# Kernel optimization log

Hardware: AMD Instinct MI355X
Metric: run time of the kernel (lower is better)

Reference implementation:

```python
import math
import jax, jax.numpy as jnp
import numpy as np

STEP = 0.1
EPS = 1e-12


def _laplacian(src, dst, n):
    # dense symmetric-normalized Laplacian from COO edge list (symmetrized, 0/1 weights)
    A = jnp.zeros((n, n), dtype=jnp.float32).at[src, dst].set(1.0)
    A = jnp.maximum(A, A.T)
    deg = A.sum(axis=1)
    dinv = jnp.where(deg > 0, 1.0 / jnp.sqrt(jnp.maximum(deg, 1e-12)), 0.0)
    return jnp.eye(n, dtype=jnp.float32) - dinv[:, None] * A * dinv[None, :]


def _filter_bank(L, bs):
    # rational band-pass bank centered at b in arange(0,2.1,STEP):
    # D_b = sqrt(2)*a * inv((L - b I)^4 + a I),  a = (STEP/2)^4
    n = L.shape[0]
    a = (STEP / 2.0) ** 4
    I = jnp.eye(n, dtype=L.dtype)

    def one(b):
        M1 = L - b * I
        P2 = M1 @ M1
        P4 = P2 @ P2
        return math.sqrt(2.0) * a * jnp.linalg.inv(P4 + a * I)

    return jax.vmap(one)(bs)  # [F, n, n]


def _cdist_mean(e):
    # mean pairwise euclidean distance, safe sqrt on the zero diagonal
    d2 = jnp.sum((e[:, None, :] - e[None, :, :]) ** 2, axis=-1)
    d = jnp.sqrt(jnp.where(d2 > 0, d2, 1.0))
    return jnp.where(d2 > 0, d, 0.0).mean()


def setup_inputs() -> dict:
    key = jax.random.key(0)
    k1, k2, k3, k4, k5 = jax.random.split(key, 5)
    B, N, F0, R, E = 64, 128, 32, 1118, 512
    return {
        "x": jax.random.normal(k1, (B, N, F0), dtype=jnp.float32),
        "random_signal": jax.random.normal(k2, (B, N, R), dtype=jnp.float32),
        "C": jax.random.normal(k3, (21, 1), dtype=jnp.float32),
        "edge_src": jax.random.randint(k4, (B, E), 0, N),
        "edge_dst": jax.random.randint(k5, (B, E), 0, N),
        "num_classes": 4,
    }


def reference(x, random_signal, C, edge_src, edge_dst, num_classes):
    B, N, _ = x.shape
    R = random_signal.shape[-1]
    # torch.normal(0, sqrt(1/R)) random signal concatenated to features
    feats = jnp.concatenate([x, random_signal * math.sqrt(1.0 / R)], axis=-1)  # [B,N,F0+R]
    bs = jnp.arange(0.0, 2.1, STEP, dtype=jnp.float32)  # [21]
    Cn = C / jnp.maximum(jnp.linalg.norm(C, axis=0, keepdims=True), EPS)  # F.normalize(C, dim=0)

    def per_graph(src, dst, xg):
        L = _laplacian(src, dst, N)
        D = _filter_bank(L, bs)                      # [F,N,N]
        L_hat = jnp.einsum('fnm,f->nm', D, Cn[:, 0])  # D.permute(1,2,0) @ C, squeezed
        A_hat = jnp.eye(N, dtype=xg.dtype) - L_hat
        y = A_hat @ xg                                # [N, F0+R]
        z = y / jnp.maximum(jnp.linalg.norm(y, axis=1, keepdims=True), EPS)
        logits = z @ z.T                              # decode_all on normalized x
        sp = -jnp.abs(logits).sum() / (N * N)         # -||logits||_1 / n^2
        return y.mean(axis=0), sp

    emb, sp_terms = jax.vmap(per_graph)(edge_src, edge_dst, feats)  # [B,D], [B]

    # faithful repeated in-loop division: s_{i+1} = (s_i + t_i)/B  =>  sum_i t_i * B^{-(B-i)}
    i = jnp.arange(B, dtype=jnp.float32)
    w = jnp.exp(-(B - i) * jnp.log(float(B)))
    sparsity_fwd = jnp.sum(sp_terms * w)

    # labels y = arange(B) % num_classes; one positive group (class members) and
    # one negative group (non-members) per class
    idx = np.arange(B)
    hl1 = jnp.float32(0.0)
    hl2 = jnp.float32(0.0)
    for c in range(num_classes):
        pos = jnp.asarray(idx[idx % num_classes == c])
        neg = jnp.asarray(idx[idx % num_classes != c])
        beta = 1.0 / num_classes + 1e-13  # one group per class
        hl1 = hl1 + (-_cdist_mean(emb[neg])) / beta
        hl2 = hl2 + _cdist_mean(emb[pos])

    Fk = C.shape[0]
    dims = jnp.sqrt(jnp.float32(Fk))
    c_l1 = jnp.sum(jnp.abs(C), axis=0)
    c_l2 = jnp.maximum(jnp.linalg.norm(C, axis=0), EPS)
    sparsity_c = jnp.mean((dims - c_l1 / c_l2) / (dims - 1.0))

    return sparsity_c + hl2 + hl1 + sparsity_fwd
```

## Files before the change

### kernel.cpp

```cpp
#include <hip/hip_runtime.h>
#include <math.h>

#define NN 128
#define SM 129
#define RS 132
#define SS 17
#define SD 130
#define EP 132

typedef double d4 __attribute__((ext_vector_type(4)));

__global__ __launch_bounds__(512, 1) void k1_lap_pow2(
    const int* __restrict__ src, const int* __restrict__ dst,
    int E, float* __restrict__ Lout, double* __restrict__ L2) {
  extern __shared__ float smf[];
  float* dinv = smf + NN * SM;
  const int g   = blockIdx.x;
  const int tid = threadIdx.x;
  const int wv = tid >> 6, ln = tid & 63;
  const int m  = ln & 15, kq = ln >> 4;

  int rIdx[4], cIdx[4];
  {
    d4 z = {0.0, 0.0, 0.0, 0.0};
    d4 pr = __builtin_amdgcn_mfma_f64_16x16x4f64((double)m, 1.0, z, 0, 0, 0);
    d4 pc = __builtin_amdgcn_mfma_f64_16x16x4f64(1.0, (double)m, z, 0, 0, 0);
#pragma unroll
    for (int r = 0; r < 4; ++r) {
      rIdx[r] = ((int)(pr[r] * 0.25 + 0.5)) & 15;
      cIdx[r] = ((int)(pc[r] * 0.25 + 0.5)) & 15;
    }
  }

  for (int e = tid; e < NN * NN; e += 512) {
    int i = e >> 7, j = e & 127;
    smf[i * SM + j] = 0.f;
  }
  __syncthreads();
  const int* s = src + (size_t)g * E;
  const int* d = dst + (size_t)g * E;
  for (int e = tid; e < E; e += 512) {
    int a = s[e], b = d[e];
    smf[a * SM + b] = 1.f;
    smf[b * SM + a] = 1.f;
  }
  __syncthreads();
  if (tid < NN) {
    float acc = 0.f;
    for (int j = 0; j < NN; ++j) acc += smf[tid * SM + j];
    dinv[tid] = (acc > 0.f) ? (float)(1.0 / sqrt((double)acc)) : 0.f;
  }
  __syncthreads();
  float* Lg = Lout + (size_t)g * NN * NN;
  for (int e = tid; e < NN * NN; e += 512) {
    int i = e >> 7, j = e & 127;
    float v = ((i == j) ? 1.f : 0.f) - dinv[i] * dinv[j] * smf[i * SM + j];
    Lg[e] = v;
    smf[i * SM + j] = v;
  }
  __syncthreads();

  d4 acc[8];
#pragma unroll
  for (int cb = 0; cb < 8; ++cb) {
    acc[cb][0] = 0.0; acc[cb][1] = 0.0; acc[cb][2] = 0.0; acc[cb][3] = 0.0;
  }
  for (int kc = 0; kc < 32; ++kc) {
    double a = (double)smf[(16 * wv + m) * SM + 4 * kc + kq];
#pragma unroll
    for (int cb = 0; cb < 8; ++cb) {
      double b = (double)smf[(4 * kc + kq) * SM + 16 * cb + m];
      acc[cb] = __builtin_amdgcn_mfma_f64_16x16x4f64(a, b, acc[cb], 0, 0, 0);
    }
  }
  double* out = L2 + (size_t)g * NN * NN;
#pragma unroll
  for (int cb = 0; cb < 8; ++cb)
#pragma unroll
    for (int r = 0; r < 4; ++r)
      out[(16 * wv + rIdx[r]) * NN + 16 * cb + cIdx[r]] = acc[cb][r];
}

__global__ __launch_bounds__(512, 1) void k1_pow34(
    const float* __restrict__ L, const double* __restrict__ L2,
    double* __restrict__ L3, double* __restrict__ L4) {
  extern __shared__ double Bs[];
  const int bid = blockIdx.x;
  const int g = bid >> 1, job = bid & 1;
  const int tid = threadIdx.x;
  const int wv = tid >> 6, ln = tid & 63;
  const int m  = ln & 15, kq = ln >> 4;

  int rIdx[4], cIdx[4];
  {
    d4 z = {0.0, 0.0, 0.0, 0.0};
    d4 pr = __builtin_amdgcn_mfma_f64_16x16x4f64((double)m, 1.0, z, 0, 0, 0);
    d4 pc = __builtin_amdgcn_mfma_f64_16x16x4f64(1.0, (double)m, z, 0, 0, 0);
#pragma unroll
    for (int r = 0; r < 4; ++r) {
      rIdx[r] = ((int)(pr[r] * 0.25 + 0.5)) & 15;
      cIdx[r] = ((int)(pc[r] * 0.25 + 0.5)) & 15;
    }
  }

  const float*  Lg  = L  + (size_t)g * NN * NN;
  const double* L2g = L2 + (size_t)g * NN * NN;
  if (job == 0) {
    for (int e = tid; e < NN * NN; e += 512) {
      int i = e >> 7, j = e & 127;
      Bs[i * SD + j] = (double)Lg[e];
    }
  } else {
    for (int e = tid; e < NN * NN; e += 512) {
      int i = e >> 7, j = e & 127;
      Bs[i * SD + j] = L2g[e];
    }
  }
  __syncthreads();

  d4 acc[8];
#pragma unroll
  for (int cb = 0; cb < 8; ++cb) {
    acc[cb][0] = 0.0; acc[cb][1] = 0.0; acc[cb][2] = 0.0; acc[cb][3] = 0.0;
  }
  for (int kc = 0; kc < 32; ++kc) {
    double a = L2g[(16 * wv + m) * NN + 4 * kc + kq];
#pragma unroll
    for (int cb = 0; cb < 8; ++cb) {
      double b = Bs[(4 * kc + kq) * SD + 16 * cb + m];
      acc[cb] = __builtin_amdgcn_mfma_f64_16x16x4f64(a, b, acc[cb], 0, 0, 0);
    }
  }
  double* out = (job == 0 ? L3 : L4) + (size_t)g * NN * NN;
#pragma unroll
  for (int cb = 0; cb < 8; ++cb)
#pragma unroll
    for (int r = 0; r < 4; ++r)
      out[(16 * wv + rIdx[r]) * NN + 16 * cb + cIdx[r]] = acc[cb][r];
}

__global__ __launch_bounds__(512, 4) void k2_filter(
    const float* __restrict__ L, const double* __restrict__ L2,
    const double* __restrict__ L3, const double* __restrict__ L4,
    const float* __restrict__ C, int NF, float* __restrict__ W) {
  extern __shared__ char smraw[];
  double* Rp  = (double*)smraw;
  double* Scd = (double*)(smraw + 16 * RS * 8);
  double* Pv  = (double*)(smraw + 16 * RS * 8 + 8 * 16 * SS * 8);

  const int bid = blockIdx.x;
  const int g = bid / NF, f = bid % NF;
  const int tid = threadIdx.x;
  const int wv = tid >> 6, ln = tid & 63;
  const int m  = ln & 15, kq = ln >> 4;
  double* S = Scd + wv * 16 * SS;

  double csum = 0.0;
  for (int q = 0; q < NF; ++q) { double c = (double)C[q]; csum += c * c; }
  double cn = sqrt(csum); if (cn < 1e-12) cn = 1e-12;
  const double a4 = 6.25e-6;
  const double coef = 1.4142135623730951 * a4 * ((double)C[f] / cn);
  const float  bf = (float)((double)f * 0.1);
  const double bb = (double)bf;
  const double c3 = -4.0 * bb;
  const double c2 = 6.0 * bb * bb;
  const double c1 = -4.0 * bb * bb * bb;
  const double c0 = bb * bb * bb * bb + a4;

  int rIdx[4], cIdx[4];
  {
    d4 z = {0.0, 0.0, 0.0, 0.0};
    d4 pr = __builtin_amdgcn_mfma_f64_16x16x4f64((double)m, 1.0, z, 0, 0, 0);
    d4 pc = __builtin_amdgcn_mfma_f64_16x16x4f64(1.0, (double)m, z, 0, 0, 0);
#pragma unroll
    for (int r = 0; r < 4; ++r) {
      rIdx[r] = ((int)(pr[r] * 0.25 + 0.5)) & 15;
      cIdx[r] = ((int)(pc[r] * 0.25 + 0.5)) & 15;
    }
  }

  const float*  Lg  = L  + (size_t)g * NN * NN;
  const double* L2g = L2 + (size_t)g * NN * NN;
  const double* L3g = L3 + (size_t)g * NN * NN;
  const double* L4g = L4 + (size_t)g * NN * NN;
  d4 T[8];
#pragma unroll
  for (int cb = 0; cb < 8; ++cb)
#pragma unroll
    for (int r = 0; r < 4; ++r) {
      int i = 16 * wv + rIdx[r], j = 16 * cb + cIdx[r];
      int idx = i * NN + j;
      double v = L4g[idx];
      v = fma(c3, L3g[idx], v);
      v = fma(c2, L2g[idx], v);
      v = fma(c1, (double)Lg[idx], v);
      if (i == j) v += c0;
      T[cb][r] = v;
    }

#pragma unroll 1
  for (int t = 0; t < 8; ++t) {
    if (wv == t) {
#pragma unroll
      for (int cb = 0; cb < 8; ++cb)
#pragma unroll
        for (int r = 0; r < 4; ++r)
          Rp[rIdx[r] * RS + 16 * cb + cIdx[r]] = T[cb][r];
    }
    __syncthreads();

    if (wv == t) {
      double sr[4];
#pragma unroll
      for (int r = 0; r < 4; ++r) sr[r] = Rp[(4 * r + kq) * RS + 16 * t + m];
#pragma unroll
      for (int k = 0; k < 16; ++k) {
        const int kr = k >> 2, kl = k & 3;
        double pv   = __shfl(sr[kr], 16 * kl + k);
        double rowv = __shfl(sr[kr], 16 * kl + m);
        double cv[4];
#pragma unroll
        for (int r = 0; r < 4; ++r) cv[r] = __shfl(sr[r], 16 * kq + k);
        double dp = 1.0 / pv;
#pragma unroll
        for (int r = 0; r < 4; ++r) {
          int i = 4 * r + kq;
          double nv;
          if (i == k)      nv = (m == k) ? dp : rowv * dp;
          else if (m == k) nv = -cv[r] * dp;
          else             nv = fma(-(cv[r] * dp), rowv, sr[r]);
          sr[r] = nv;
        }
      }
#pragma unroll
      for (int r = 0; r < 4; ++r) Pv[(4 * r + kq) * SS + m] = sr[r];
    }
    __syncthreads();

#pragma unroll
    for (int cb = 0; cb < 8; ++cb) {
      if (cb != t) continue;
      if (wv == t) {
#pragma unroll
        for (int r = 0; r < 4; ++r) T[cb][r] = Pv[rIdx[r] * SS + cIdx[r]];
      } else {
#pragma unroll
        for (int r = 0; r < 4; ++r) S[rIdx[r] * SS + cIdx[r]] = T[cb][r];
        __builtin_amdgcn_wave_barrier();
        d4 ncv = {0.0, 0.0, 0.0, 0.0};
#pragma unroll
        for (int kc = 0; kc < 4; ++kc) {
          double a = S[m * SS + 4 * kc + kq];
          double b = -Pv[(4 * kc + kq) * SS + m];
          ncv = __builtin_amdgcn_mfma_f64_16x16x4f64(a, b, ncv, 0, 0, 0);
        }
        T[cb] = ncv;
        __builtin_amdgcn_wave_barrier();
#pragma unroll
        for (int r = 0; r < 4; ++r) S[rIdx[r] * SS + cIdx[r]] = T[cb][r];
      }
    }
    __builtin_amdgcn_wave_barrier();

    const double* asrc = (wv == t) ? Pv : S;
#pragma unroll
    for (int cb = 0; cb < 8; ++cb) {
      if (cb == t) continue;
      d4 acc;
      if (wv == t) { acc[0] = 0.0; acc[1] = 0.0; acc[2] = 0.0; acc[3] = 0.0; }
      else         { acc = T[cb]; }
#pragma unroll
      for (int kc = 0; kc < 4; ++kc) {
        double a = asrc[m * SS + 4 * kc + kq];
        double b = Rp[(4 * kc + kq) * RS + 16 * cb + m];
        acc = __builtin_amdgcn_mfma_f64_16x16x4f64(a, b, acc, 0, 0, 0);
      }
      T[cb] = acc;
    }
    __syncthreads();
  }

  float* Wg = W + (size_t)g * NN * NN;
#pragma unroll
  for (int cb = 0; cb < 8; ++cb)
#pragma unroll
    for (int r = 0; r < 4; ++r)
      atomicAdd(&Wg[(16 * wv + rIdx[r]) * NN + 16 * cb + cIdx[r]],
                (float)(coef * T[cb][r]));
}

__global__ __launch_bounds__(512, 1) void k3_fused(
    const float* __restrict__ x, const float* __restrict__ rs,
    const float* __restrict__ W, float* __restrict__ G,
    float* __restrict__ emb, int F0, int R, int DTOT, int NCH,
    float rscale) {
  extern __shared__ float sm3[];
  float* ldsW = sm3;
  float* ldsX = sm3 + NN * SM;
  const int bid = blockIdx.x;
  const int g = bid / NCH;
  const int c = bid % NCH;
  const int d0 = c * 128;
  const int tid = threadIdx.x, tr = tid >> 4, tc = tid & 15;

  const float* Wg = W + (size_t)g * NN * NN;
  for (int e = tid; e < NN * NN; e += 512) {
    int k = e >> 7, i = e & 127;
    ldsW[k * SM + i] = Wg[e];
  }
  const float* xg = x + (size_t)g * NN * F0;
  const float* rg = rs + (size_t)g * NN * R;
  for (int e = tid; e < NN * NN; e += 512) {
    int k = e >> 7, dl = e & 127;
    int d = d0 + dl;
    float v = 0.f;
    if (d < DTOT) v = (d < F0) ? xg[k * F0 + d] : rg[k * R + (d - F0)] * rscale;
    ldsX[k * SM + dl] = v;
  }
  __syncthreads();

  float acc[4][8];
#pragma unroll
  for (int v = 0; v < 4; ++v)
#pragma unroll
    for (int u = 0; u < 8; ++u) acc[v][u] = 0.f;
  for (int k = 0; k < NN; ++k) {
    float wvv[4], xv[8];
#pragma unroll
    for (int v = 0; v < 4; ++v) wvv[v] = ldsW[k * SM + 4 * tr + v];
#pragma unroll
    for (int u = 0; u < 8; ++u) xv[u] = ldsX[k * SM + tc + 16 * u];
#pragma unroll
    for (int v = 0; v < 4; ++v)
#pragma unroll
      for (int u = 0; u < 8; ++u) acc[v][u] = fmaf(wvv[v], xv[u], acc[v][u]);
  }
#pragma unroll
  for (int v = 0; v < 4; ++v)
#pragma unroll
    for (int u = 0; u < 8; ++u)
      acc[v][u] = ldsX[(4 * tr + v) * SM + tc + 16 * u] - acc[v][u];
  __syncthreads();

#pragma unroll
  for (int v = 0; v < 4; ++v)
#pragma unroll
    for (int u = 0; u < 8; ++u)
      ldsW[(tc + 16 * u) * SM + 4 * tr + v] = acc[v][u];
#pragma unroll
  for (int u = 0; u < 8; ++u) {
    float s = 0.f;
#pragma unroll
    for (int v = 0; v < 4; ++v) s += acc[v][u];
    ldsX[tr * EP + tc + 16 * u] = s;
  }
  __syncthreads();

  float gg[4][8];
#pragma unroll
  for (int v = 0; v < 4; ++v)
#pragma unroll
    for (int u = 0; u < 8; ++u) gg[v][u] = 0.f;
  for (int dl = 0; dl < NN; ++dl) {
    float av[4], bv[8];
#pragma unroll
    for (int v = 0; v < 4; ++v) av[v] = ldsW[dl * SM + 4 * tr + v];
#pragma unroll
    for (int u = 0; u < 8; ++u) bv[u] = ldsW[dl * SM + tc + 16 * u];
#pragma unroll
    for (int v = 0; v < 4; ++v)
#pragma unroll
      for (int u = 0; u < 8; ++u) gg[v][u] = fmaf(av[v], bv[u], gg[v][u]);
  }
  float* Gg = G + (size_t)g * NN * NN;
#pragma unroll
  for (int v = 0; v < 4; ++v)
#pragma unroll
    for (int u = 0; u < 8; ++u)
      atomicAdd(&Gg[(4 * tr + v) * NN + tc + 16 * u], gg[v][u]);

  if (tid < 128) {
    int d = d0 + tid;
    if (d < DTOT) {
      float s = 0.f;
      for (int tt = 0; tt < 32; ++tt) s += ldsX[tt * EP + tid];
      emb[(size_t)g * 1152 + d] = s * (1.f / 128.f);
    }
  }
}

__global__ __launch_bounds__(256) void k45_fused(
    const float* __restrict__ G, double* __restrict__ spt,
    const float* __restrict__ emb, float* __restrict__ Dm, int DTOT) {
  __shared__ float inr[NN];
  __shared__ double red[4];
  const int bid = blockIdx.x, tid = threadIdx.x;
  if (bid < 64) {
    const int g = bid;
    const float* Gg = G + (size_t)g * NN * NN;
    if (tid < NN) {
      float n = sqrtf(fmaxf(Gg[tid * NN + tid], 0.f));
      inr[tid] = 1.f / fmaxf(n, 1e-12f);
    }
    __syncthreads();
    double s = 0.0;
    for (int e = tid; e < NN * NN; e += 256) {
      int i = e >> 7, j = e & 127;
      s += (double)(fabsf(Gg[e]) * inr[i] * inr[j]);
    }
    for (int off = 32; off; off >>= 1) s += __shfl_down(s, off);
    int wave = tid >> 6, lane = tid & 63;
    if (lane == 0) red[wave] = s;
    __syncthreads();
    if (tid == 0) spt[g] = -(red[0] + red[1] + red[2] + red[3]) / (double)(NN * NN);
  } else {
    const int i = bid - 64;
    const int wv = tid >> 6, l = tid & 63;
    float ei[18];
#pragma unroll
    for (int s = 0; s < 18; ++s) {
      int d = l + 64 * s;
      ei[s] = (d < DTOT) ? emb[(size_t)i * 1152 + d] : 0.f;
    }
    for (int jj = 0; jj < 16; ++jj) {
      int j = 4 * jj + wv;
      float acc = 0.f;
#pragma unroll
      for (int s = 0; s < 18; ++s) {
        int d = l + 64 * s;
        if (d < DTOT) {
          float df = ei[s] - emb[(size_t)j * 1152 + d];
          acc = fmaf(df, df, acc);
        }
      }
      for (int off = 32; off; off >>= 1) acc += __shfl_down(acc, off);
      if (l == 0) Dm[i * 64 + j] = (acc > 0.f) ? sqrtf(acc) : 0.f;
    }
  }
}

__global__ __launch_bounds__(64) void k5b_final(
    const float* __restrict__ Dm, const double* __restrict__ spt,
    const float* __restrict__ C, int NF,
    const int* __restrict__ ncls, float* __restrict__ out) {
  const int lane = threadIdx.x;
  const int nc = ncls[0];
  double spf = spt[lane] * exp(-((double)(64 - lane)) * log(64.0));
  for (int off = 32; off; off >>= 1) spf += __shfl_down(spf, off);

  double hl1 = 0.0, hl2 = 0.0;
  const double beta = 1.0 / (double)nc + 1e-13;
  for (int cc = 0; cc < nc; ++cc) {
    bool ip = (lane % nc) == cc;
    double ps = 0.0, ns = 0.0;
    for (int j = 0; j < 64; ++j) {
      double dv = (double)Dm[lane * 64 + j];
      bool jp = (j % nc) == cc;
      if (ip && jp) ps += dv;
      if (!ip && !jp) ns += dv;
    }
    for (int off = 32; off; off >>= 1) {
      ps += __shfl_down(ps, off);
      ns += __shfl_down(ns, off);
    }
    int npos = 0;
    for (int q = 0; q < 64; ++q) if (q % nc == cc) npos++;
    int nneg = 64 - npos;
    hl2 += ps / ((double)npos * (double)npos);
    hl1 += -(ns / ((double)nneg * (double)nneg)) / beta;
  }
  if (lane == 0) {
    double l1 = 0.0, l2 = 0.0;
    for (int q = 0; q < NF; ++q) { double cv = (double)C[q]; l1 += fabs(cv); l2 += cv * cv; }
    l2 = sqrt(l2); if (l2 < 1e-12) l2 = 1e-12;
    double dims = sqrt((double)NF);
    double sc = (dims - l1 / l2) / (dims - 1.0);
    out[0] = (float)(sc + hl2 + hl1 + spf);
  }
}

extern "C" void kernel_launch(void* const* d_in, const int* in_sizes, int n_in,
                              void* d_out, int out_size, void* d_ws, size_t ws_size,
                              hipStream_t stream) {
  (void)n_in; (void)out_size; (void)ws_size;
  const float* x    = (const float*)d_in[0];
  const float* rs   = (const float*)d_in[1];
  const float* C    = (const float*)d_in[2];
  const int*   esrc = (const int*)d_in[3];
  const int*   edst = (const int*)d_in[4];
  const int*   ncls = (const int*)d_in[5];
  float* out = (float*)d_out;

  const int F0   = in_sizes[0] / (64 * 128);
  const int R    = in_sizes[1] / (64 * 128);
  const int NF   = in_sizes[2];
  const int E    = in_sizes[3] / 64;
  const int DTOT = F0 + R;
  const int NCH  = (DTOT + 127) / 128;
  const float rscale = (float)(1.0 / sqrt((double)R));

  char* ws = (char*)d_ws;
  size_t off = 0;
  float*  L    = (float*)(ws + off);  off += (size_t)64 * NN * NN * 4;
  float*  W    = (float*)(ws + off);  off += (size_t)64 * NN * NN * 4;
  float*  G    = (float*)(ws + off);  off += (size_t)64 * NN * NN * 4;
  double* L2d  = (double*)(ws + off); off += (size_t)64 * NN * NN * 8;
  double* L3d  = (double*)(ws + off); off += (size_t)64 * NN * NN * 8;
  double* L4d  = (double*)(ws + off); off += (size_t)64 * NN * NN * 8;
  float*  emb  = (float*)(ws + off);  off += (size_t)64 * 1152 * 4;
  double* spt  = (double*)(ws + off); off += (size_t)64 * 8;
  float*  Dm   = (float*)(ws + off);  off += (size_t)64 * 64 * 4;

  hipMemsetAsync(W, 0, (size_t)64 * NN * NN * 4, stream);
  hipMemsetAsync(G, 0, (size_t)64 * NN * NN * 4, stream);

  const int lds1 = (NN * SM + NN) * 4;
  const int ldsp = NN * SD * 8;
  const int lds2 = 16 * RS * 8 + 8 * 16 * SS * 8 + 16 * SS * 8;
  const int lds3 = (NN * SM) * 4 * 2;
  hipFuncSetAttribute((const void*)k1_lap_pow2, hipFuncAttributeMaxDynamicSharedMemorySize, lds1);
  hipFuncSetAttribute((const void*)k1_pow34,    hipFuncAttributeMaxDynamicSharedMemorySize, ldsp);
  hipFuncSetAttribute((const void*)k2_filter,   hipFuncAttributeMaxDynamicSharedMemorySize, lds2);
  hipFuncSetAttribute((const void*)k3_fused,    hipFuncAttributeMaxDynamicSharedMemorySize, lds3);

  k1_lap_pow2<<<64, 512, lds1, stream>>>(esrc, edst, E, L, L2d);
  k1_pow34<<<128, 512, ldsp, stream>>>(L, L2d, L3d, L4d);
  k2_filter<<<64 * NF, 512, lds2, stream>>>(L, L2d, L3d, L4d, C, NF, W);
  k3_fused<<<64 * NCH, 512, lds3, stream>>>(x, rs, W, G, emb, F0, R, DTOT, NCH, rscale);
  k45_fused<<<128, 256, 0, stream>>>(G, spt, emb, Dm, DTOT);
  k5b_final<<<1, 64, 0, stream>>>(Dm, spt, C, NF, ncls, out);
}
```

Baseline: 646.4 us.

## Use FP64 MFMA for both GEMMs in fused projection kernel

Replaces the scalar FP32 FMA register-tiled matmuls in k3_fused (W·X and the Gram matrix Y·Yᵀ) with FP64 16x16x4 MFMA instructions. Output coordinates are recovered by an MFMA-based index-discovery trick reused from k1. The embedding column sum now reads from the transposed Y tile instead of a partial-sum buffer. This adds float-to-double conversions and runs on the FP64 matrix pipe, trading scalar FMA throughput for matrix-core throughput.

```diff
diff --git a/kernel.cpp b/kernel.cpp
--- a/kernel.cpp
+++ b/kernel.cpp
@@ -6,7 +6,6 @@
 #define RS 132
 #define SS 17
 #define SD 130
-#define EP 132
 
 typedef double d4 __attribute__((ext_vector_type(4)));
 
@@ -301,89 +300,92 @@
   const int g = bid / NCH;
   const int c = bid % NCH;
   const int d0 = c * 128;
-  const int tid = threadIdx.x, tr = tid >> 4, tc = tid & 15;
+  const int tid = threadIdx.x;
+  const int wv = tid >> 6, ln = tid & 63;
+  const int m  = ln & 15, kq = ln >> 4;
+
+  int rIdx[4], cIdx[4];
+  {
+    d4 z = {0.0, 0.0, 0.0, 0.0};
+    d4 pr = __builtin_amdgcn_mfma_f64_16x16x4f64((double)m, 1.0, z, 0, 0, 0);
+    d4 pc = __builtin_amdgcn_mfma_f64_16x16x4f64(1.0, (double)m, z, 0, 0, 0);
+#pragma unroll
+    for (int r = 0; r < 4; ++r) {
+      rIdx[r] = ((int)(pr[r] * 0.25 + 0.5)) & 15;
+      cIdx[r] = ((int)(pc[r] * 0.25 + 0.5)) & 15;
+    }
+  }
 
   const float* Wg = W + (size_t)g * NN * NN;
   for (int e = tid; e < NN * NN; e += 512) {
-    int k = e >> 7, i = e & 127;
-    ldsW[k * SM + i] = Wg[e];
+    int i = e >> 7, j = e & 127;
+    ldsW[i * SM + j] = Wg[e];
   }
   const float* xg = x + (size_t)g * NN * F0;
   const float* rg = rs + (size_t)g * NN * R;
   for (int e = tid; e < NN * NN; e += 512) {
-    int k = e >> 7, dl = e & 127;
+    int i = e >> 7, dl = e & 127;
     int d = d0 + dl;
     float v = 0.f;
-    if (d < DTOT) v = (d < F0) ? xg[k * F0 + d] : rg[k * R + (d - F0)] * rscale;
-    ldsX[k * SM + dl] = v;
-  }
-  __syncthreads();
-
-  float acc[4][8];
-#pragma unroll
-  for (int v = 0; v < 4; ++v)
-#pragma unroll
-    for (int u = 0; u < 8; ++u) acc[v][u] = 0.f;
-  for (int k = 0; k < NN; ++k) {
-    float wvv[4], xv[8];
-#pragma unroll
-    for (int v = 0; v < 4; ++v) wvv[v] = ldsW[k * SM + 4 * tr + v];
-#pragma unroll
-    for (int u = 0; u < 8; ++u) xv[u] = ldsX[k * SM + tc + 16 * u];
-#pragma unroll
-    for (int v = 0; v < 4; ++v)
-#pragma unroll
-      for (int u = 0; u < 8; ++u) acc[v][u] = fmaf(wvv[v], xv[u], acc[v][u]);
-  }
-#pragma unroll
-  for (int v = 0; v < 4; ++v)
-#pragma unroll
-    for (int u = 0; u < 8; ++u)
-      acc[v][u] = ldsX[(4 * tr + v) * SM + tc + 16 * u] - acc[v][u];
-  __syncthreads();
-
-#pragma unroll
-  for (int v = 0; v < 4; ++v)
-#pragma unroll
-    for (int u = 0; u < 8; ++u)
-      ldsW[(tc + 16 * u) * SM + 4 * tr + v] = acc[v][u];
-#pragma unroll
-  for (int u = 0; u < 8; ++u) {
-    float s = 0.f;
-#pragma unroll
-    for (int v = 0; v < 4; ++v) s += acc[v][u];
-    ldsX[tr * EP + tc + 16 * u] = s;
-  }
-  __syncthreads();
-
-  float gg[4][8];
-#pragma unroll
-  for (int v = 0; v < 4; ++v)
-#pragma unroll
-    for (int u = 0; u < 8; ++u) gg[v][u] = 0.f;
-  for (int dl = 0; dl < NN; ++dl) {
-    float av[4], bv[8];
-#pragma unroll
-    for (int v = 0; v < 4; ++v) av[v] = ldsW[dl * SM + 4 * tr + v];
-#pragma unroll
-    for (int u = 0; u < 8; ++u) bv[u] = ldsW[dl * SM + tc + 16 * u];
-#pragma unroll
-    for (int v = 0; v < 4; ++v)
-#pragma unroll
-      for (int u = 0; u < 8; ++u) gg[v][u] = fmaf(av[v], bv[u], gg[v][u]);
+    if (d < DTOT) v = (d < F0) ? xg[i * F0 + d] : rg[i * R + (d - F0)] * rscale;
+    ldsX[i * SM + dl] = v;
+  }
+  __syncthreads();
+
+  d4 T[8];
+#pragma unroll
+  for (int cb = 0; cb < 8; ++cb) {
+    T[cb][0] = 0.0; T[cb][1] = 0.0; T[cb][2] = 0.0; T[cb][3] = 0.0;
+  }
+  for (int kc = 0; kc < 32; ++kc) {
+    double a = (double)ldsW[(16 * wv + m) * SM + 4 * kc + kq];
+#pragma unroll
+    for (int cb = 0; cb < 8; ++cb) {
+      double b = (double)ldsX[(4 * kc + kq) * SM + 16 * cb + m];
+      T[cb] = __builtin_amdgcn_mfma_f64_16x16x4f64(a, b, T[cb], 0, 0, 0);
+    }
+  }
+#pragma unroll
+  for (int cb = 0; cb < 8; ++cb)
+#pragma unroll
+    for (int r = 0; r < 4; ++r)
+      T[cb][r] = (double)ldsX[(16 * wv + rIdx[r]) * SM + 16 * cb + cIdx[r]]
+                 - T[cb][r];
+  __syncthreads();
+
+#pragma unroll
+  for (int cb = 0; cb < 8; ++cb)
+#pragma unroll
+    for (int r = 0; r < 4; ++r)
+      ldsW[(16 * wv + rIdx[r]) * SM + 16 * cb + cIdx[r]] = (float)T[cb][r];
+  __syncthreads();
+
+  d4 Ga[8];
+#pragma unroll
+  for (int cb = 0; cb < 8; ++cb) {
+    Ga[cb][0] = 0.0; Ga[cb][1] = 0.0; Ga[cb][2] = 0.0; Ga[cb][3] = 0.0;
+  }
+  for (int kc = 0; kc < 32; ++kc) {
+    double a = (double)ldsW[(16 * wv + m) * SM + 4 * kc + kq];
+#pragma unroll
+    for (int cb = 0; cb < 8; ++cb) {
+      double b = (double)ldsW[(16 * cb + m) * SM + 4 * kc + kq];
+      Ga[cb] = __builtin_amdgcn_mfma_f64_16x16x4f64(a, b, Ga[cb], 0, 0, 0);
+    }
   }
   float* Gg = G + (size_t)g * NN * NN;
 #pragma unroll
-  for (int v = 0; v < 4; ++v)
-#pragma unroll
-    for (int u = 0; u < 8; ++u)
-      atomicAdd(&Gg[(4 * tr + v) * NN + tc + 16 * u], gg[v][u]);
+  for (int cb = 0; cb < 8; ++cb)
+#pragma unroll
+    for (int r = 0; r < 4; ++r)
+      atomicAdd(&Gg[(16 * wv + rIdx[r]) * NN + 16 * cb + cIdx[r]],
+                (float)Ga[cb][r]);
 
   if (tid < 128) {
     int d = d0 + tid;
     if (d < DTOT) {
       float s = 0.f;
-      for (int tt = 0; tt < 32; ++tt) s += ldsX[tt * EP + tid];
+      for (int i = 0; i < NN; ++i) s += ldsW[i * SM + tid];
       emb[(size_t)g * 1152 + d] = s * (1.f / 128.f);
     }
   }
```

New measurement: 662.6 us. 2.5% more time.
